# Performance work log

Hardware: AMD Instinct MI355X
Metric: run time of the kernel (lower is better)

Reference implementation:

```python
import jax, jax.numpy as jnp
import numpy as np

N = 50000
E = 800000
IN_DIM = 128
HID = 64
OUT_DIM = 128
NEG_SLOPE = 0.2  # PyG GATConv default


def _add_self_loops(src, dst, edge_attr, n):
    # PyG GATConv(add_self_loops=True) with edge_dim uses fill_value='mean':
    # self-loop edge_attr = mean of edge_attr of incoming edges per node.
    deg = jax.ops.segment_sum(jnp.ones((src.shape[0],), edge_attr.dtype), dst, num_segments=n)
    loop_attr = jax.ops.segment_sum(edge_attr, dst, num_segments=n) / jnp.maximum(deg, 1.0)[:, None]
    loop = jnp.arange(n, dtype=src.dtype)
    return (jnp.concatenate([src, loop]), jnp.concatenate([dst, loop]),
            jnp.concatenate([edge_attr, loop_attr], axis=0))


def _gat_conv(x, src, dst, edge_attr, W, We, a_src, a_dst, a_edge, bias, heads, out_dim, concat, n):
    src, dst, edge_attr = _add_self_loops(src, dst, edge_attr, n)
    h = (x @ W).reshape(n, heads, out_dim)                      # [N,H,D]
    he = (edge_attr @ We).reshape(-1, heads, out_dim)           # [E',H,D]
    alpha_src = jnp.einsum('nhd,hd->nh', h, a_src)
    alpha_dst = jnp.einsum('nhd,hd->nh', h, a_dst)
    alpha_edge = jnp.einsum('ehd,hd->eh', he, a_edge)
    alpha = jax.nn.leaky_relu(alpha_src[src] + alpha_dst[dst] + alpha_edge, NEG_SLOPE)  # [E',H]
    # segment softmax over edges grouped by destination node
    amax = jax.ops.segment_max(alpha, dst, num_segments=n)
    amax = jnp.where(jnp.isfinite(amax), amax, 0.0)
    ex = jnp.exp(alpha - amax[dst])
    denom = jax.ops.segment_sum(ex, dst, num_segments=n)
    coef = ex / (denom[dst] + 1e-16)                            # [E',H]
    msg = h[src] * coef[:, :, None]                             # [E',H,D]
    out = jax.ops.segment_sum(msg, dst, num_segments=n)         # [N,H,D]
    out = out.reshape(n, heads * out_dim) if concat else out.mean(axis=1)
    return out + bias


def setup_inputs() -> dict:
    key = jax.random.key(0)
    ks = jax.random.split(key, 16)
    s = 0.05
    inp = {
        'x': jax.random.normal(ks[0], (N, IN_DIM), jnp.float32),
        'edge_index': jax.random.randint(ks[1], (2, E), 0, N, dtype=jnp.int64),
        'edge_attr': jax.random.normal(ks[2], (E, 2), jnp.float32),
        # gat1: heads=4, concat -> out 4*HID
        'W1': jax.random.normal(ks[3], (IN_DIM, 4 * HID), jnp.float32) * s,
        'We1': jax.random.normal(ks[4], (2, 4 * HID), jnp.float32) * s,
        'asrc1': jax.random.normal(ks[5], (4, HID), jnp.float32) * s,
        'adst1': jax.random.normal(ks[6], (4, HID), jnp.float32) * s,
        'aedge1': jax.random.normal(ks[7], (4, HID), jnp.float32) * s,
        'b1': jnp.zeros((4 * HID,), jnp.float32),
        # gat2: heads=1, concat=False -> out OUT_DIM
        'W2': jax.random.normal(ks[8], (4 * HID, OUT_DIM), jnp.float32) * s,
        'We2': jax.random.normal(ks[9], (2, OUT_DIM), jnp.float32) * s,
        'asrc2': jax.random.normal(ks[10], (1, OUT_DIM), jnp.float32) * s,
        'adst2': jax.random.normal(ks[11], (1, OUT_DIM), jnp.float32) * s,
        'aedge2': jax.random.normal(ks[12], (1, OUT_DIM), jnp.float32) * s,
        'b2': jnp.zeros((OUT_DIM,), jnp.float32),
    }
    return inp


def reference(x, edge_index, edge_attr, W1, We1, asrc1, adst1, aedge1, b1,
              W2, We2, asrc2, adst2, aedge2, b2):
    src, dst = edge_index[0], edge_index[1]
    # dropout layers are identity in eval mode
    h = _gat_conv(x, src, dst, edge_attr, W1, We1, asrc1, adst1, aedge1, b1,
                  heads=4, out_dim=HID, concat=True, n=x.shape[0])
    h = jax.nn.elu(h)
    out = _gat_conv(h, src, dst, edge_attr, W2, We2, asrc2, adst2, aedge2, b2,
                    heads=1, out_dim=OUT_DIM, concat=False, n=x.shape[0])
    return out
```

## Files before the change

### kernel.cpp

```cpp
#include <hip/hip_runtime.h>
#include <hip/hip_bf16.h>

#define NN 50000
#define EE 800000
#define SCAN_B 2048
#define NB ((NN + SCAN_B - 1) / SCAN_B)
#define LOG2E 1.44269504088896340736f
#define GB1 1564


typedef short bf16x8 __attribute__((ext_vector_type(8)));
typedef float f32x4  __attribute__((ext_vector_type(4)));

__device__ __forceinline__ unsigned short f2bf(float f) {
    unsigned b = __float_as_uint(f);
    b += 0x7fffu + ((b >> 16) & 1u);
    return (unsigned short)(b >> 16);
}
__device__ __forceinline__ float2 bfpair(unsigned u) {
    return make_float2(__uint_as_float(u << 16), __uint_as_float(u & 0xffff0000u));
}

__global__ void k_prep(const float* __restrict__ We1, const float* __restrict__ ae1,
                       const float* __restrict__ We2, const float* __restrict__ ae2,
                       float* __restrict__ v,
                       const float* __restrict__ W1, unsigned short* __restrict__ W1t,
                       const float* __restrict__ W2, unsigned short* __restrict__ W2t,
                       const int* __restrict__ ei, int* __restrict__ idg,
                       int* __restrict__ rank,
                       const float* __restrict__ x, unsigned short* __restrict__ xb) {
    int bid = blockIdx.x, t = threadIdx.x;
    if (bid == 0) {
        if (t < 8) {
            int c = t >> 2, h = t & 3;
            float s = 0.f;
            for (int d = 0; d < 64; d++) s += We1[c * 256 + h * 64 + d] * ae1[h * 64 + d];
            v[c * 4 + h] = s * LOG2E;
        } else if (t < 10) {
            int c = t - 8;
            float s = 0.f;
            for (int d = 0; d < 128; d++) s += We2[c * 128 + d] * ae2[d];
            v[8 + c] = s * LOG2E;
        }
    } else if (bid <= 256) {
        int idx = (bid - 1) * 256 + t;
        if (idx < 32768) {
            int k = idx >> 8, n = idx & 255;
            W1t[n * 128 + k] = f2bf(W1[idx]);
        } else {
            int i = idx - 32768;
            int k = i >> 7, n = i & 127;
            W2t[n * 256 + k] = f2bf(W2[i]);
        }
    } else if (bid <= 256 + 3125) {
        int e = (bid - 257) * 256 + t;
        if (e < EE) rank[e] = atomicAdd(&idg[ei[EE + e]], 1);
    } else {
        int i = (bid - 3382) * 256 + t;
        if (i < NN * 128 / 4) {
            float4 vv = ((const float4*)x)[i];
            ushort4 o;
            o.x = f2bf(vv.x); o.y = f2bf(vv.y); o.z = f2bf(vv.z); o.w = f2bf(vv.w);
            ((ushort4*)xb)[i] = o;
        }
    }
}

__global__ void k_scan12(const int* __restrict__ idg, int* __restrict__ rowptr,
                         int* __restrict__ bsum, int* __restrict__ boff,
                         int* __restrict__ ticket) {
    __shared__ int sh[512];
    int t = threadIdx.x;
    int base = blockIdx.x * SCAN_B + t * 4;
    int v[4]; int s = 0;
    #pragma unroll
    for (int j = 0; j < 4; j++) {
        int i = base + j;
        v[j] = (i < NN) ? idg[i] : 0;
        s += v[j];
    }
    sh[t] = s;
    __syncthreads();
    for (int off = 1; off < 512; off <<= 1) {
        int a = (t >= off) ? sh[t - off] : 0;
        __syncthreads();
        sh[t] += a;
        __syncthreads();
    }
    int run = sh[t] - s;
    #pragma unroll
    for (int j = 0; j < 4; j++) {
        int i = base + j;
        if (i < NN) rowptr[i] = run;
        run += v[j];
    }
    if (t == 511) bsum[blockIdx.x] = sh[511];
    __syncthreads();
    __threadfence();
    if (t == 0) {
        int done = atomicAdd(ticket, 1);
        if (done == NB - 1) {
            __threadfence();
            int acc = 0;
            for (int b = 0; b < NB; b++) { boff[b] = acc; acc += bsum[b]; }
            rowptr[NN] = acc;
        }
    }
}

__global__ void k_scan3(int* __restrict__ rowptr, const int* __restrict__ boff) {
    int t = threadIdx.x;
    int i = blockIdx.x * SCAN_B + t * 4;
    int off = boff[blockIdx.x];
    #pragma unroll
    for (int j = 0; j < 4; j++)
        if (i + j < NN) rowptr[i + j] += off;
}

template <int K, int NT, int H>
__device__ __forceinline__ void gemm_body(int bx, int by,
                                          const unsigned short* __restrict__ A,
                                          const unsigned short* __restrict__ Bt,
                                          unsigned short* __restrict__ C,
                                          const float* __restrict__ avs,
                                          const float* __restrict__ avd,
                                          float* __restrict__ asrc,
                                          float* __restrict__ adst,
                                          int M, int N) {
    int wave = threadIdx.x >> 6, lane = threadIdx.x & 63;
    int l16 = lane & 15, quad = lane >> 4;
    int m0 = by * 128 + wave * 32;
    int n0 = bx * (NT * 16);

    f32x4 acc[2][NT];
    #pragma unroll
    for (int mt = 0; mt < 2; mt++)
        #pragma unroll
        for (int nt = 0; nt < NT; nt++)
            acc[mt][nt] = (f32x4){0.f, 0.f, 0.f, 0.f};

    int ar0 = min(m0 + l16, M - 1);
    int ar1 = min(m0 + 16 + l16, M - 1);
    const unsigned short* a0 = A + (size_t)ar0 * K + quad * 8;
    const unsigned short* a1 = A + (size_t)ar1 * K + quad * 8;
    const unsigned short* bp = Bt + (size_t)(n0 + l16) * K + quad * 8;

    #pragma unroll
    for (int k0 = 0; k0 < K; k0 += 32) {
        bf16x8 af0 = *(const bf16x8*)(a0 + k0);
        bf16x8 af1 = *(const bf16x8*)(a1 + k0);
        #pragma unroll
        for (int nt = 0; nt < NT; nt++) {
            bf16x8 bf = *(const bf16x8*)(bp + (size_t)nt * 16 * K + k0);
            acc[0][nt] = __builtin_amdgcn_mfma_f32_16x16x32_bf16(af0, bf, acc[0][nt], 0, 0, 0);
            acc[1][nt] = __builtin_amdgcn_mfma_f32_16x16x32_bf16(af1, bf, acc[1][nt], 0, 0, 0);
        }
    }

    #pragma unroll
    for (int mt = 0; mt < 2; mt++)
        #pragma unroll
        for (int reg = 0; reg < 4; reg++) {
            int row = m0 + mt * 16 + quad * 4 + reg;
            if (row < M) {
                #pragma unroll
                for (int nt = 0; nt < NT; nt++)
                    C[(size_t)row * N + n0 + nt * 16 + l16] = f2bf(acc[mt][nt][reg]);
            }
        }

    float ws[NT], wd[NT];
    #pragma unroll
    for (int nt = 0; nt < NT; nt++) {
        ws[nt] = avs[n0 + nt * 16 + l16] * LOG2E;
        wd[nt] = avd[n0 + nt * 16 + l16] * LOG2E;
    }
    int hh = n0 >> 6;
    #pragma unroll
    for (int mt = 0; mt < 2; mt++)
        #pragma unroll
        for (int reg = 0; reg < 4; reg++) {
            int row = m0 + mt * 16 + quad * 4 + reg;
            float s1 = 0.f, s2 = 0.f;
            #pragma unroll
            for (int nt = 0; nt < NT; nt++) {
                float c = acc[mt][nt][reg];
                s1 += c * ws[nt];
                s2 += c * wd[nt];
            }
            #pragma unroll
            for (int off = 1; off < 16; off <<= 1) {
                s1 += __shfl_xor(s1, off);
                s2 += __shfl_xor(s2, off);
            }
            if (l16 == 0 && row < M) {
                asrc[row * H + hh] = s1;
                adst[row * H + hh] = s2;
            }
        }
}

__global__ __launch_bounds__(256) void k_sg(const unsigned short* __restrict__ xb,
                       const unsigned short* __restrict__ W1t,
                       unsigned short* __restrict__ h1b,
                       const float* __restrict__ as1, const float* __restrict__ ad1,
                       float* __restrict__ asrc1, float* __restrict__ adst1,
                       const int* __restrict__ ei, const float* __restrict__ eattr,
                       const int* __restrict__ rowptr, const int* __restrict__ rank,
                       int2* __restrict__ slot) {
    int bid = blockIdx.x;
    if (bid < GB1) {
        gemm_body<128, 4, 4>(bid & 3, bid >> 2, xb, W1t, h1b, as1, ad1,
                             asrc1, adst1, NN, 256);
    } else {
        int e = (bid - GB1) * 256 + threadIdx.x;
        if (e >= EE) return;
        int s = ei[e], d = ei[EE + e];
        int p = rowptr[d] + rank[e];
        float2 a = ((const float2*)eattr)[e];
        unsigned a0 = f2bf(a.x), a1 = f2bf(a.y);
        slot[p] = make_int2(s, (int)(a0 | (a1 << 16)));
    }
}

__global__ __launch_bounds__(256) void k_gemm2(const unsigned short* __restrict__ A,
                       const unsigned short* __restrict__ Bt,
                       unsigned short* __restrict__ C,
                       const float* __restrict__ avs, const float* __restrict__ avd,
                       float* __restrict__ asrc, float* __restrict__ adst) {
    gemm_body<256, 8, 1>(0, blockIdx.x, A, Bt, C, avs, avd, asrc, adst, NN, 128);
}

__global__ __launch_bounds__(256) void k_agg1(const int* __restrict__ rowptr,
                       const int2* __restrict__ slot, const float* __restrict__ asrc,
                       const float* __restrict__ adst, const float* __restrict__ v,
                       const unsigned short* __restrict__ hb, const float* __restrict__ b1,
                       unsigned short* __restrict__ h2b) {
    int node = blockIdx.x * 4 + (threadIdx.x >> 6);
    if (node >= NN) return;
    int lane = threadIdx.x & 63;
    int h2 = lane >> 5;
    int hl = lane & 31;
    int hd = hl >> 3;
    int beg = rowptr[node], end = rowptr[node + 1];
    float pd = adst[node * 4 + hd];
    float vh0 = v[hd], vh1 = v[4 + hd];
    float acc[8] = {};
    float den = 0.f, s0 = 0.f, s1 = 0.f;
    const unsigned short* hbq = hb + hl * 8;

    int cnt = end - beg;
    int safeLast = max(end - 1, 0);
    int mend = beg + (cnt & ~1);

    int2 sl0 = slot[min(beg + h2, safeLast)];
    int2 sl1 = slot[min(beg + 2 + h2, safeLast)];

    auto body = [&](int2 cur) {
        int s = cur.x;
        float2 a = bfpair((unsigned)cur.y);
        float al = asrc[s * 4 + hd] + pd + a.x * vh0 + a.y * vh1;
        al = (al > 0.f) ? al : 0.2f * al;
        float e = __builtin_amdgcn_exp2f(al);
        s0 += a.x; s1 += a.y; den += e;
        uint4 r = *(const uint4*)(hbq + (size_t)s * 256);
        float2 p;
        p = bfpair(r.x); acc[0] += e * p.x; acc[1] += e * p.y;
        p = bfpair(r.y); acc[2] += e * p.x; acc[3] += e * p.y;
        p = bfpair(r.z); acc[4] += e * p.x; acc[5] += e * p.y;
        p = bfpair(r.w); acc[6] += e * p.x; acc[7] += e * p.y;
    };

    #pragma unroll 2
    for (int pb = beg; pb < mend; pb += 2) {
        int2 cur = sl0;
        sl0 = sl1;
        sl1 = slot[min(pb + 4 + h2, safeLast)];
        body(cur);
    }
    if (h2 == 0 && mend < end) body(sl0);

    #pragma unroll
    for (int k = 0; k < 8; k++) acc[k] += __shfl_down(acc[k], 32);
    den += __shfl_xor(den, 32);
    s0  += __shfl_xor(s0, 32);
    s1  += __shfl_xor(s1, 32);

    float dg = fmaxf((float)cnt, 1.0f);
    float als = asrc[node * 4 + hd] + pd + (s0 / dg) * vh0 + (s1 / dg) * vh1;
    als = (als > 0.f) ? als : 0.2f * als;
    float exs = __builtin_amdgcn_exp2f(als);
    den += exs;

    if (h2 == 0) {
        uint4 r = *(const uint4*)(hbq + (size_t)node * 256);
        float2 p;
        p = bfpair(r.x); acc[0] += exs * p.x; acc[1] += exs * p.y;
        p = bfpair(r.y); acc[2] += exs * p.x; acc[3] += exs * p.y;
        p = bfpair(r.z); acc[4] += exs * p.x; acc[5] += exs * p.y;
        p = bfpair(r.w); acc[6] += exs * p.x; acc[7] += exs * p.y;
        float inv = 1.f / (den + 1e-16f);
        short ov[8];
        #pragma unroll
        for (int k = 0; k < 8; k++) {
            float va = acc[k] * inv + b1[hl * 8 + k];
            va = (va > 0.f) ? va : __expf(va) - 1.f;
            ov[k] = (short)f2bf(va);
        }
        bf16x8 o8 = {ov[0], ov[1], ov[2], ov[3], ov[4], ov[5], ov[6], ov[7]};
        *(bf16x8*)(h2b + (size_t)node * 256 + hl * 8) = o8;
    }
}

__global__ __launch_bounds__(256) void k_agg2(const int* __restrict__ rowptr,
                       const int2* __restrict__ slot, const float* __restrict__ asrc,
                       const float* __restrict__ adst, const float* __restrict__ v,
                       const unsigned short* __restrict__ gb, const float* __restrict__ b2,
                       float* __restrict__ outp) {
    int node = blockIdx.x * 4 + (threadIdx.x >> 6);
    if (node >= NN) return;
    int lane = threadIdx.x & 63;
    int q  = lane >> 4;
    int ql = lane & 15;
    int beg = rowptr[node], end = rowptr[node + 1];
    float ad = adst[node];
    float v0 = v[0], v1 = v[1];
    float acc[8] = {};
    float den = 0.f, s0 = 0.f, s1 = 0.f;
    const unsigned short* gbq = gb + ql * 8;

    int cnt = end - beg;
    int safeLast = max(end - 1, 0);
    int mend = beg + (cnt & ~3);

    int2 sl0 = slot[min(beg + q, safeLast)];
    int2 sl1 = slot[min(beg + 4 + q, safeLast)];

    auto body = [&](int2 cur) {
        int s = cur.x;
        float2 a = bfpair((unsigned)cur.y);
        float al = asrc[s] + ad + a.x * v0 + a.y * v1;
        al = (al > 0.f) ? al : 0.2f * al;
        float e = __builtin_amdgcn_exp2f(al);
        s0 += a.x; s1 += a.y; den += e;
        uint4 r = *(const uint4*)(gbq + (size_t)s * 128);
        float2 p;
        p = bfpair(r.x); acc[0] += e * p.x; acc[1] += e * p.y;
        p = bfpair(r.y); acc[2] += e * p.x; acc[3] += e * p.y;
        p = bfpair(r.z); acc[4] += e * p.x; acc[5] += e * p.y;
        p = bfpair(r.w); acc[6] += e * p.x; acc[7] += e * p.y;
    };

    #pragma unroll 2
    for (int pb = beg; pb < mend; pb += 4) {
        int2 cur = sl0;
        sl0 = sl1;
        sl1 = slot[min(pb + 8 + q, safeLast)];
        body(cur);
    }
    if (mend + q < end) body(sl0);

    #pragma unroll
    for (int k = 0; k < 8; k++) {
        acc[k] += __shfl_down(acc[k], 32);
        acc[k] += __shfl_down(acc[k], 16);
    }
    den += __shfl_xor(den, 16); den += __shfl_xor(den, 32);
    s0  += __shfl_xor(s0, 16);  s0  += __shfl_xor(s0, 32);
    s1  += __shfl_xor(s1, 16);  s1  += __shfl_xor(s1, 32);

    float dg = fmaxf((float)cnt, 1.0f);
    float als = asrc[node] + ad + (s0 / dg) * v0 + (s1 / dg) * v1;
    als = (als > 0.f) ? als : 0.2f * als;
    float exs = __builtin_amdgcn_exp2f(als);
    den += exs;

    if (q == 0) {
        uint4 r = *(const uint4*)(gbq + (size_t)node * 128);
        float2 p;
        p = bfpair(r.x); acc[0] += exs * p.x; acc[1] += exs * p.y;
        p = bfpair(r.y); acc[2] += exs * p.x; acc[3] += exs * p.y;
        p = bfpair(r.z); acc[4] += exs * p.x; acc[5] += exs * p.y;
        p = bfpair(r.w); acc[6] += exs * p.x; acc[7] += exs * p.y;
        float inv = 1.f / (den + 1e-16f);
        float4 o0, o1;
        o0.x = acc[0] * inv + b2[ql * 8 + 0];
        o0.y = acc[1] * inv + b2[ql * 8 + 1];
        o0.z = acc[2] * inv + b2[ql * 8 + 2];
        o0.w = acc[3] * inv + b2[ql * 8 + 3];
        o1.x = acc[4] * inv + b2[ql * 8 + 4];
        o1.y = acc[5] * inv + b2[ql * 8 + 5];
        o1.z = acc[6] * inv + b2[ql * 8 + 6];
        o1.w = acc[7] * inv + b2[ql * 8 + 7];
        *(float4*)(outp + (size_t)node * 128 + ql * 8)     = o0;
        *(float4*)(outp + (size_t)node * 128 + ql * 8 + 4) = o1;
    }
}

extern "C" void kernel_launch(void* const* d_in, const int* in_sizes, int n_in,
                              void* d_out, int out_size, void* d_ws, size_t ws_size,
                              hipStream_t stream) {
    const float* x     = (const float*)d_in[0];
    const int*   ei    = (const int*)d_in[1];
    const float* eattr = (const float*)d_in[2];
    const float* W1    = (const float*)d_in[3];
    const float* We1   = (const float*)d_in[4];
    const float* as1   = (const float*)d_in[5];
    const float* ad1   = (const float*)d_in[6];
    const float* ae1   = (const float*)d_in[7];
    const float* b1    = (const float*)d_in[8];
    const float* W2    = (const float*)d_in[9];
    const float* We2   = (const float*)d_in[10];
    const float* as2   = (const float*)d_in[11];
    const float* ad2   = (const float*)d_in[12];
    const float* ae2   = (const float*)d_in[13];
    const float* b2    = (const float*)d_in[14];
    float* out = (float*)d_out;

    int* idg    = (int*)d_ws;
    int* ticket = idg + NN;
    int* rank   = ticket + 16;
    int* rowptr = rank + EE;
    int* bsum   = rowptr + NN + 16;
    int* boff   = bsum + 32;
    int2* slot  = (int2*)(boff + 32);
    float* asrc1 = (float*)(slot + EE);
    float* adst1 = asrc1 + 4 * NN;
    float* asrc2 = adst1 + 4 * NN;
    float* adst2 = asrc2 + NN;
    float* vbuf  = adst2 + NN;
    unsigned short* ub = (unsigned short*)(((uintptr_t)(vbuf + 64) + 63) & ~(uintptr_t)63);
    unsigned short* x_bf  = ub;
    unsigned short* W1t   = x_bf + (size_t)NN * 128;
    unsigned short* W2t   = W1t + 32768;
    unsigned short* h1_bf = W2t + 32768;
    unsigned short* h2_bf = h1_bf + (size_t)NN * 256;
    unsigned short* g2_bf = h2_bf + (size_t)NN * 256;

    hipMemsetAsync(idg, 0, (size_t)(NN + 16) * sizeof(int), stream);

    k_prep<<<9632, 256, 0, stream>>>(We1, ae1, We2, ae2, vbuf, W1, W1t, W2, W2t,
                                     ei, idg, rank, x, x_bf);
    k_scan12<<<NB, 512, 0, stream>>>(idg, rowptr, bsum, boff, ticket);
    k_scan3<<<NB, 512, 0, stream>>>(rowptr, boff);

    k_sg<<<GB1 + 3125, 256, 0, stream>>>(x_bf, W1t, h1_bf, as1, ad1,
                                         asrc1, adst1, ei, eattr, rowptr, rank, slot);

    k_agg1<<<(NN + 3) / 4, 256, 0, stream>>>(rowptr, slot, asrc1, adst1, vbuf,
                                             h1_bf, b1, h2_bf);

    k_gemm2<<<(NN + 127) / 128, 256, 0, stream>>>(h2_bf, W2t, g2_bf, as2, ad2,
                                                  asrc2, adst2);
    k_agg2<<<(NN + 3) / 4, 256, 0, stream>>>(rowptr, slot, asrc2, adst2, vbuf + 8,
                                             g2_bf, b2, out);
}
```

Measured before the change: 305.5 us.

## Fuse layer-2 GEMM into layer-1 aggregation and drop scan fixup kernel

Layer-1 aggregation now keeps each block's four ELU outputs in shared memory and multiplies them by W2 with MFMA, writing the layer-2 features directly. It also computes the layer-2 attention logits from precomputed W2·a vectors, so the separate gemm2 kernel and the 50000x256 intermediate round trip through memory go away. The scan's third pass is removed; consumers add the per-block offset boff themselves. In exchange, a 16x16 MFMA tile is computed with only 4 valid rows, wasting matrix throughput, and the aggregation kernel gains a block-wide barrier.

```diff
diff --git a/kernel.cpp b/kernel.cpp
--- a/kernel.cpp
+++ b/kernel.cpp
@@ -12,6 +12,9 @@
 typedef short bf16x8 __attribute__((ext_vector_type(8)));
 typedef float f32x4  __attribute__((ext_vector_type(4)));
 
+__device__ __forceinline__ float bf2f(unsigned short u) {
+    return __uint_as_float(((unsigned)u) << 16);
+}
 __device__ __forceinline__ unsigned short f2bf(float f) {
     unsigned b = __float_as_uint(f);
     b += 0x7fffu + ((b >> 16) & 1u);
@@ -24,6 +27,8 @@
 __global__ void k_prep(const float* __restrict__ We1, const float* __restrict__ ae1,
                        const float* __restrict__ We2, const float* __restrict__ ae2,
                        float* __restrict__ v,
+                       const float* __restrict__ as2, const float* __restrict__ ad2,
+                       float* __restrict__ w2s, float* __restrict__ w2d,
                        const float* __restrict__ W1, unsigned short* __restrict__ W1t,
                        const float* __restrict__ W2, unsigned short* __restrict__ W2t,
                        const int* __restrict__ ei, int* __restrict__ idg,
@@ -42,6 +47,17 @@
             for (int d = 0; d < 128; d++) s += We2[c * 128 + d] * ae2[d];
             v[8 + c] = s * LOG2E;
         }
+        {
+            float ss = 0.f, sd = 0.f;
+            const float* wr = W2 + t * 128;
+            for (int j = 0; j < 128; j++) {
+                float w = wr[j];
+                ss += w * as2[j];
+                sd += w * ad2[j];
+            }
+            w2s[t] = ss * LOG2E;
+            w2d[t] = sd * LOG2E;
+        }
     } else if (bid <= 256) {
         int idx = (bid - 1) * 256 + t;
         if (idx < 32768) {
@@ -91,7 +107,7 @@
     #pragma unroll
     for (int j = 0; j < 4; j++) {
         int i = base + j;
-        if (i < NN) rowptr[i] = run;
+        if (i <= NN) rowptr[i] = run;
         run += v[j];
     }
     if (t == 511) bsum[blockIdx.x] = sh[511];
@@ -103,18 +119,8 @@
             __threadfence();
             int acc = 0;
             for (int b = 0; b < NB; b++) { boff[b] = acc; acc += bsum[b]; }
-            rowptr[NN] = acc;
-        }
-    }
-}
-
-__global__ void k_scan3(int* __restrict__ rowptr, const int* __restrict__ boff) {
-    int t = threadIdx.x;
-    int i = blockIdx.x * SCAN_B + t * 4;
-    int off = boff[blockIdx.x];
-    #pragma unroll
-    for (int j = 0; j < 4; j++)
-        if (i + j < NN) rowptr[i + j] += off;
+        }
+    }
 }
 
 template <int K, int NT, int H>
@@ -206,8 +212,8 @@
                        const float* __restrict__ as1, const float* __restrict__ ad1,
                        float* __restrict__ asrc1, float* __restrict__ adst1,
                        const int* __restrict__ ei, const float* __restrict__ eattr,
-                       const int* __restrict__ rowptr, const int* __restrict__ rank,
-                       int2* __restrict__ slot) {
+                       const int* __restrict__ rowptr, const int* __restrict__ boff,
+                       const int* __restrict__ rank, int2* __restrict__ slot) {
     int bid = blockIdx.x;
     if (bid < GB1) {
         gemm_body<128, 4, 4>(bid & 3, bid >> 2, xb, W1t, h1b, as1, ad1,
@@ -216,33 +222,31 @@
         int e = (bid - GB1) * 256 + threadIdx.x;
         if (e >= EE) return;
         int s = ei[e], d = ei[EE + e];
-        int p = rowptr[d] + rank[e];
+        int p = rowptr[d] + boff[d >> 11] + rank[e];
         float2 a = ((const float2*)eattr)[e];
         unsigned a0 = f2bf(a.x), a1 = f2bf(a.y);
         slot[p] = make_int2(s, (int)(a0 | (a1 << 16)));
     }
 }
 
-__global__ __launch_bounds__(256) void k_gemm2(const unsigned short* __restrict__ A,
-                       const unsigned short* __restrict__ Bt,
-                       unsigned short* __restrict__ C,
-                       const float* __restrict__ avs, const float* __restrict__ avd,
-                       float* __restrict__ asrc, float* __restrict__ adst) {
-    gemm_body<256, 8, 1>(0, blockIdx.x, A, Bt, C, avs, avd, asrc, adst, NN, 128);
-}
-
 __global__ __launch_bounds__(256) void k_agg1(const int* __restrict__ rowptr,
+                       const int* __restrict__ boff,
                        const int2* __restrict__ slot, const float* __restrict__ asrc,
                        const float* __restrict__ adst, const float* __restrict__ v,
                        const unsigned short* __restrict__ hb, const float* __restrict__ b1,
-                       unsigned short* __restrict__ h2b) {
-    int node = blockIdx.x * 4 + (threadIdx.x >> 6);
-    if (node >= NN) return;
+                       const unsigned short* __restrict__ W2t,
+                       const float* __restrict__ w2s, const float* __restrict__ w2d,
+                       unsigned short* __restrict__ g2b,
+                       float* __restrict__ asrc2, float* __restrict__ adst2) {
+    __shared__ unsigned short shh[4][256];
+    int wv = threadIdx.x >> 6;
+    int node = blockIdx.x * 4 + wv;
     int lane = threadIdx.x & 63;
     int h2 = lane >> 5;
     int hl = lane & 31;
     int hd = hl >> 3;
-    int beg = rowptr[node], end = rowptr[node + 1];
+    int beg = rowptr[node] + boff[node >> 11];
+    int end = rowptr[node + 1] + boff[(node + 1) >> 11];
     float pd = adst[node * 4 + hd];
     float vh0 = v[hd], vh1 = v[4 + hd];
     float acc[8] = {};
@@ -292,6 +296,7 @@
     float exs = __builtin_amdgcn_exp2f(als);
     den += exs;
 
+    float p_s = 0.f, p_d = 0.f;
     if (h2 == 0) {
         uint4 r = *(const uint4*)(hbq + (size_t)node * 256);
         float2 p;
@@ -306,13 +311,51 @@
             float va = acc[k] * inv + b1[hl * 8 + k];
             va = (va > 0.f) ? va : __expf(va) - 1.f;
             ov[k] = (short)f2bf(va);
+            float vr = bf2f((unsigned short)ov[k]);
+            p_s += vr * w2s[hl * 8 + k];
+            p_d += vr * w2d[hl * 8 + k];
         }
         bf16x8 o8 = {ov[0], ov[1], ov[2], ov[3], ov[4], ov[5], ov[6], ov[7]};
-        *(bf16x8*)(h2b + (size_t)node * 256 + hl * 8) = o8;
+        *(bf16x8*)(&shh[wv][hl * 8]) = o8;
+    }
+    #pragma unroll
+    for (int off = 1; off < 32; off <<= 1) {
+        p_s += __shfl_xor(p_s, off);
+        p_d += __shfl_xor(p_d, off);
+    }
+    if (lane == 0) {
+        asrc2[node] = p_s;
+        adst2[node] = p_d;
+    }
+
+    __syncthreads();
+
+    {
+        int l16 = lane & 15, quad = lane >> 4;
+        int nb = blockIdx.x * 4;
+        #pragma unroll
+        for (int t = 0; t < 2; t++) {
+            int n0 = (wv * 2 + t) * 16;
+            f32x4 c = (f32x4){0.f, 0.f, 0.f, 0.f};
+            const unsigned short* bp = W2t + (size_t)(n0 + l16) * 256 + quad * 8;
+            const unsigned short* ap = &shh[l16 & 3][quad * 8];
+            #pragma unroll
+            for (int k0 = 0; k0 < 256; k0 += 32) {
+                bf16x8 af = *(const bf16x8*)(ap + k0);
+                bf16x8 bf = *(const bf16x8*)(bp + k0);
+                c = __builtin_amdgcn_mfma_f32_16x16x32_bf16(af, bf, c, 0, 0, 0);
+            }
+            if (quad == 0) {
+                #pragma unroll
+                for (int reg = 0; reg < 4; reg++)
+                    g2b[(size_t)(nb + reg) * 128 + n0 + l16] = f2bf(c[reg]);
+            }
+        }
     }
 }
 
 __global__ __launch_bounds__(256) void k_agg2(const int* __restrict__ rowptr,
+                       const int* __restrict__ boff,
                        const int2* __restrict__ slot, const float* __restrict__ asrc,
                        const float* __restrict__ adst, const float* __restrict__ v,
                        const unsigned short* __restrict__ gb, const float* __restrict__ b2,
@@ -322,7 +365,8 @@
     int lane = threadIdx.x & 63;
     int q  = lane >> 4;
     int ql = lane & 15;
-    int beg = rowptr[node], end = rowptr[node + 1];
+    int beg = rowptr[node] + boff[node >> 11];
+    int end = rowptr[node + 1] + boff[(node + 1) >> 11];
     float ad = adst[node];
     float v0 = v[0], v1 = v[1];
     float acc[8] = {};
@@ -429,29 +473,29 @@
     float* asrc2 = adst1 + 4 * NN;
     float* adst2 = asrc2 + NN;
     float* vbuf  = adst2 + NN;
-    unsigned short* ub = (unsigned short*)(((uintptr_t)(vbuf + 64) + 63) & ~(uintptr_t)63);
+    float* w2s   = vbuf + 64;
+    float* w2d   = w2s + 256;
+    unsigned short* ub = (unsigned short*)(((uintptr_t)(w2d + 256) + 63) & ~(uintptr_t)63);
     unsigned short* x_bf  = ub;
     unsigned short* W1t   = x_bf + (size_t)NN * 128;
     unsigned short* W2t   = W1t + 32768;
     unsigned short* h1_bf = W2t + 32768;
-    unsigned short* h2_bf = h1_bf + (size_t)NN * 256;
-    unsigned short* g2_bf = h2_bf + (size_t)NN * 256;
+    unsigned short* g2_bf = h1_bf + (size_t)NN * 256;
 
     hipMemsetAsync(idg, 0, (size_t)(NN + 16) * sizeof(int), stream);
 
-    k_prep<<<9632, 256, 0, stream>>>(We1, ae1, We2, ae2, vbuf, W1, W1t, W2, W2t,
-                                     ei, idg, rank, x, x_bf);
+    k_prep<<<9632, 256, 0, stream>>>(We1, ae1, We2, ae2, vbuf, as2, ad2, w2s, w2d,
+                                     W1, W1t, W2, W2t, ei, idg, rank, x, x_bf);
     k_scan12<<<NB, 512, 0, stream>>>(idg, rowptr, bsum, boff, ticket);
-    k_scan3<<<NB, 512, 0, stream>>>(rowptr, boff);
 
     k_sg<<<GB1 + 3125, 256, 0, stream>>>(x_bf, W1t, h1_bf, as1, ad1,
-                                         asrc1, adst1, ei, eattr, rowptr, rank, slot);
-
-    k_agg1<<<(NN + 3) / 4, 256, 0, stream>>>(rowptr, slot, asrc1, adst1, vbuf,
-                                             h1_bf, b1, h2_bf);
-
-    k_gemm2<<<(NN + 127) / 128, 256, 0, stream>>>(h2_bf, W2t, g2_bf, as2, ad2,
-                                                  asrc2, adst2);
-    k_agg2<<<(NN + 3) / 4, 256, 0, stream>>>(rowptr, slot, asrc2, adst2, vbuf + 8,
-                                             g2_bf, b2, out);
-}
+                                         asrc1, adst1, ei, eattr, rowptr, boff,
+                                         rank, slot);
+
+    k_agg1<<<NN / 4, 256, 0, stream>>>(rowptr, boff, slot, asrc1, adst1, vbuf,
+                                       h1_bf, b1, W2t, w2s, w2d, g2_bf,
+                                       asrc2, adst2);
+
+    k_agg2<<<(NN + 3) / 4, 256, 0, stream>>>(rowptr, boff, slot, asrc2, adst2,
+                                             vbuf + 8, g2_bf, b2, out);
+}
```

New measurement: 353.8 us. 15.8% more time.
